# Kernel optimization log

Hardware: AMD Instinct MI355X
Metric: run time of the kernel (lower is better)

## Reference

```python
import jax, jax.numpy as jnp
import numpy as np

N_FFT = 1024
HOP = 256
B = 8
T = 2048  # n_frames
FREQ = N_FFT // 2 + 1


def setup_inputs() -> dict:
    key = jax.random.key(0)
    k1, k2 = jax.random.split(key)
    real_stft = jax.random.normal(k1, (B, 1, T, FREQ), dtype=jnp.float32)
    imag_stft = jax.random.normal(k2, (B, 1, T, FREQ), dtype=jnp.float32)
    # Build DFT synthesis matrices (same as torch module __init__, scaled=False)
    n = np.arange(N_FFT)
    hann = (0.5 - 0.5 * np.cos(2.0 * np.pi * n / N_FFT))  # fftbins=True hann
    ang = 2.0 * np.pi * np.outer(n, n) / N_FFT            # [k, n]
    W_real = (np.cos(ang) * hann[None, :] / N_FFT).astype(np.float32)
    W_imag = (np.sin(ang) * hann[None, :] / N_FFT).astype(np.float32)
    ola_window = (hann ** 2).astype(np.float32)
    return {
        "real_stft": real_stft,
        "imag_stft": imag_stft,
        "W_real": jnp.asarray(W_real),
        "W_imag": jnp.asarray(W_imag),
        "ola_window": jnp.asarray(ola_window),
    }


def reference(real_stft, imag_stft, W_real, W_imag, ola_window):
    n_fft = W_real.shape[0]
    b, _, n_frames, _ = real_stft.shape
    # (B, T, F) -> (B, F, T)
    fr = jnp.swapaxes(real_stft[:, 0], 1, 2)
    fi = jnp.swapaxes(imag_stft[:, 0], 1, 2)
    # Hermitian extension to full spectrum (B, n_fft, T)
    full_r = jnp.concatenate([fr, jnp.flip(fr[:, 1:-1, :], axis=1)], axis=1)
    full_i = jnp.concatenate([fi, -jnp.flip(fi[:, 1:-1, :], axis=1)], axis=1)
    # 1x1-conv DFT projection: out[b,t,n] = sum_k W[k,n] * x[b,k,t]
    frames = (jnp.einsum('kn,bkt->btn', W_real, full_r)
              - jnp.einsum('kn,bkt->btn', W_imag, full_i))  # (B, T, n_fft)
    out_len = (n_frames - 1) * HOP + n_fft
    # Overlap-add fold via scatter-add
    idx = (jnp.arange(n_frames)[:, None] * HOP + jnp.arange(n_fft)[None, :]).reshape(-1)
    y = jnp.zeros((b, out_len), frames.dtype).at[:, idx].add(frames.reshape(b, -1))
    # Window-sum fold + normalization
    wsum = jnp.zeros((out_len,), frames.dtype).at[idx].add(jnp.tile(ola_window, n_frames))
    wsum = jnp.clip(wsum, 1e-11, None)
    y = y / wsum[None, :]
    half = n_fft // 2
    return y[:, half:out_len - half]
```

## Files before the change

### kernel.cpp

```cpp
#include <hip/hip_runtime.h>


#define BATCH    8
#define NFRAMES  2048
#define FREQ     513
#define OUTCOLS  524032
#define FRAMES_B ((size_t)16384 * 1024 * 2)
#define TW_OFF   FRAMES_B
#define HANN_OFF (FRAMES_B + 16384)
#define WS_NEED  (FRAMES_B + 16384 + 4096)

typedef __attribute__((ext_vector_type(2))) float f32x2;
typedef __attribute__((ext_vector_type(4))) float f32x4;
typedef __attribute__((ext_vector_type(2))) unsigned uint2v;

__device__ __forceinline__ unsigned short f2bf(float x) {
    unsigned u = __float_as_uint(x);
    return (unsigned short)((u + 0x7fffu + ((u >> 16) & 1u)) >> 16);
}

__device__ __forceinline__ f32x2 cmul(f32x2 u, f32x4 w4) {
    return (f32x2){u[0], u[0]} * (f32x2){w4[0], w4[1]}
         + (f32x2){u[1], u[1]} * (f32x2){w4[2], w4[3]};
}

__global__ __launch_bounds__(256) void table_prep(const float* __restrict__ ola,
                                                  float* __restrict__ tw4,
                                                  float* __restrict__ hann) {
    int k = blockIdx.x * 256 + threadIdx.x;
    float s, c;
    sincosf(6.283185307179586f * (float)k * (1.0f / 1024.0f), &s, &c);
    ((f32x4*)tw4)[k] = (f32x4){c, s, -s, c};
    hann[k] = sqrtf(ola[k]) * (1.0f / 1024.0f);
}

__global__ __launch_bounds__(64, 4) void ifft_wave(
    const float* __restrict__ re, const float* __restrict__ im,
    const float* __restrict__ twg, const float* __restrict__ hann,
    unsigned short* __restrict__ frames) {
    __shared__ f32x2 L[1088];

    const int l  = threadIdx.x;
    const int r0 = blockIdx.x * 2;
    const f32x4* tw4 = (const f32x4*)twg;

    const float* fre0 = re + (size_t)r0 * FREQ;
    const float* fim0 = im + (size_t)r0 * FREQ;
    const float* fre1 = fre0 + FREQ;
    const float* fim1 = fim0 + FREQ;

#define BFLY(IA, IB, IC, ID, T1, O0, O1, O2, O3)                              \
    {                                                                         \
        f32x2 apc = (IA) + (IC), amc = (IA) - (IC);                           \
        f32x2 bpd = (IB) + (ID), bmd = (IB) - (ID);                           \
        f32x2 jb  = (f32x2){-bmd[1], bmd[0]};                    \
        O0 = apc + bpd;                                                       \
        O1 = cmul(amc + jb, w1##T1);                                          \
        O2 = cmul(apc - bpd, w2##T1);                                         \
        O3 = cmul(amc - jb, w3##T1);                                          \
    }

    f32x2 s1[4][4];
#pragma unroll
    for (int j = 0; j < 4; ++j) {
        f32x2 in[4];
#pragma unroll
        for (int k = 0; k < 4; ++k) {
            int n  = l + 64 * j + 256 * k;
            int mm = (n <= 512) ? n : (1024 - n);
            float A1 = fre0[mm], B1 = fim0[mm];
            float A2 = fre1[mm], B2 = fim1[mm];
            if (n == 0 || n == 512) { B1 = 0.0f; B2 = 0.0f; }
            in[k] = (n <= 512) ? (f32x2){A1 - B2, B1 + A2}
                               : (f32x2){A1 + B2, A2 - B1};
        }
        const int t1 = l + 64 * j;
        f32x4 w1A = tw4[t1], w2A = tw4[2 * t1], w3A = tw4[3 * t1];
        BFLY(in[0], in[1], in[2], in[3], A, s1[j][0], s1[j][1], s1[j][2], s1[j][3]);
    }

    {
        const int t1 = 4 * l;
        f32x4 w1B = tw4[t1], w2B = tw4[2 * t1], w3B = tw4[3 * t1];
#pragma unroll
        for (int r = 0; r < 4; ++r) {
            f32x2 o0, o1, o2, o3;
            BFLY(s1[0][r], s1[1][r], s1[2][r], s1[3][r], B, o0, o1, o2, o3);
            int n0 = 16 * l + r;
            L[n0      + (n0 >> 4)]        = o0;
            L[n0 + 4  + ((n0 + 4) >> 4)]  = o1;
            L[n0 + 8  + ((n0 + 8) >> 4)]  = o2;
            L[n0 + 12 + ((n0 + 12) >> 4)] = o3;
        }
    }
    __syncthreads();

    f32x2 s3[4][4];
#pragma unroll
    for (int j = 0; j < 4; ++j) {
        f32x2 in[4];
#pragma unroll
        for (int k = 0; k < 4; ++k) {
            int n = l + 64 * j + 256 * k;
            in[k] = L[n + (n >> 4)];
        }
        const int t1 = ((l + 64 * j) >> 4) << 4;
        f32x4 w1C = tw4[t1], w2C = tw4[2 * t1], w3C = tw4[3 * t1];
        BFLY(in[0], in[1], in[2], in[3], C, s3[j][0], s3[j][1], s3[j][2], s3[j][3]);
    }
    __syncthreads();

    {
        const int t1 = (l >> 4) << 6;
        f32x4 w1D = tw4[t1], w2D = tw4[2 * t1], w3D = tw4[3 * t1];
#pragma unroll
        for (int r = 0; r < 4; ++r) {
            f32x2 o0, o1, o2, o3;
            BFLY(s3[0][r], s3[1][r], s3[2][r], s3[3][r], D, o0, o1, o2, o3);
            int n0 = 256 * (l >> 4) + 16 * r + (l & 15);
            int n1 = n0 + 64, n2 = n0 + 128, n3 = n0 + 192;
            L[n0 + (n0 >> 4)] = o0;
            L[n1 + (n1 >> 4)] = o1;
            L[n2 + (n2 >> 4)] = o2;
            L[n3 + (n3 >> 4)] = o3;
        }
    }
    __syncthreads();

    unsigned short* fR = frames + (size_t)r0 * 1024;
    unsigned short* fI = fR + 1024;
#pragma unroll
    for (int h = 0; h < 4; ++h) {
        int n0 = l + 64 * h;
        int n1 = n0 + 256, n2 = n0 + 512, n3 = n0 + 768;
        f32x2 a = L[n0 + (n0 >> 4)];
        f32x2 b = L[n1 + (n1 >> 4)];
        f32x2 c = L[n2 + (n2 >> 4)];
        f32x2 d = L[n3 + (n3 >> 4)];
        f32x2 apc = a + c, amc = a - c, bpd = b + d, bmd = b - d;
        f32x2 jb  = (f32x2){-bmd[1], bmd[0]};
        f32x2 y0 = apc + bpd, y1 = amc + jb, y2 = apc - bpd, y3 = amc - jb;
        float h0 = hann[n0], h1 = hann[n1], h2 = hann[n2], h3 = hann[n3];
        fR[n0] = f2bf(y0[0] * h0);  fI[n0] = f2bf(y0[1] * h0);
        fR[n1] = f2bf(y1[0] * h1);  fI[n1] = f2bf(y1[1] * h1);
        fR[n2] = f2bf(y2[0] * h2);  fI[n2] = f2bf(y2[1] * h2);
        fR[n3] = f2bf(y3[0] * h3);  fI[n3] = f2bf(y3[1] * h3);
    }
#undef BFLY
}

__global__ __launch_bounds__(256) void ola_fold4(
    const unsigned short* __restrict__ frames, const float* __restrict__ ola,
    float* __restrict__ out) {
    const int col0 = (blockIdx.x * 256 + threadIdx.x) * 4;
    if (col0 >= OUTCOLS) return;
    const int b  = blockIdx.y;
    const int s  = col0 + 512;
    const int g  = s >> 8;
    const int ls = s & 255;

    float a0 = 0.f, a1 = 0.f, a2 = 0.f, a3 = 0.f;
    float w0 = 0.f, w1 = 0.f, w2 = 0.f, w3 = 0.f;
#pragma unroll
    for (int j = 0; j < 4; ++j) {
        const int t = g - j;
        if (t >= 0 && t < NFRAMES) {
            uint2v u = *(const uint2v*)(frames + (((size_t)(b * NFRAMES + t)) << 10) + ls + 256 * j);
            a0 += __uint_as_float(u[0] << 16);
            a1 += __uint_as_float(u[0] & 0xffff0000u);
            a2 += __uint_as_float(u[1] << 16);
            a3 += __uint_as_float(u[1] & 0xffff0000u);
            f32x4 o = *(const f32x4*)(ola + ls + 256 * j);
            w0 += o[0]; w1 += o[1]; w2 += o[2]; w3 += o[3];
        }
    }
    f32x4 r = (f32x4){a0 / fmaxf(w0, 1e-11f), a1 / fmaxf(w1, 1e-11f),
                      a2 / fmaxf(w2, 1e-11f), a3 / fmaxf(w3, 1e-11f)};
    *(f32x4*)(out + (size_t)b * OUTCOLS + col0) = r;
}

__global__ __launch_bounds__(256) void istft_naive(
    const float* __restrict__ re, const float* __restrict__ im,
    const float* __restrict__ Wr, const float* __restrict__ Wi,
    const float* __restrict__ ola, float* __restrict__ out) {
    const int g = blockIdx.x + 2, b = blockIdx.y, ls = threadIdx.x;
    __shared__ float s_fr[4][FREQ];
    __shared__ float s_fi[4][FREQ];
#pragma unroll
    for (int jj = 0; jj < 4; ++jj) {
        const int t = g - jj;
        const bool valid = (t >= 0 && t < NFRAMES);
        const size_t base = ((size_t)b * NFRAMES + (valid ? t : 0)) * FREQ;
        for (int k = ls; k < FREQ; k += 256) {
            const float f = (k == 0 || k == FREQ - 1) ? 1.0f : 2.0f;
            s_fr[jj][k] = valid ? re[base + k] * f : 0.0f;
            s_fi[jj][k] = valid ? im[base + k] * f : 0.0f;
        }
    }
    __syncthreads();
    const float* wr = Wr + ls;
    const float* wi = Wi + ls;
    float acc = 0.0f;
    for (int k = 0; k < FREQ; ++k) {
        const float* wrk = wr + (size_t)k * 1024;
        const float* wik = wi + (size_t)k * 1024;
#pragma unroll
        for (int jj = 0; jj < 4; ++jj) {
            acc = fmaf(wrk[jj * 256], s_fr[jj][k], acc);
            acc = fmaf(-wik[jj * 256], s_fi[jj][k], acc);
        }
    }
    float wsv = 0.0f;
#pragma unroll
    for (int jj = 0; jj < 4; ++jj) {
        const int t = g - jj;
        if (t >= 0 && t < NFRAMES) wsv += ola[ls + jj * 256];
    }
    wsv = fmaxf(wsv, 1e-11f);
    out[(size_t)b * OUTCOLS + (g * 256 + ls - 512)] = acc / wsv;
}

extern "C" void kernel_launch(void* const* d_in, const int* in_sizes, int n_in,
                              void* d_out, int out_size, void* d_ws, size_t ws_size,
                              hipStream_t stream) {
    const float* re  = (const float*)d_in[0];
    const float* im  = (const float*)d_in[1];
    const float* Wr  = (const float*)d_in[2];
    const float* Wi  = (const float*)d_in[3];
    const float* ola = (const float*)d_in[4];
    float* out = (float*)d_out;

    if (ws_size >= WS_NEED) {
        unsigned short* frames = (unsigned short*)d_ws;
        float* tw   = (float*)((char*)d_ws + TW_OFF);
        float* hann = (float*)((char*)d_ws + HANN_OFF);
        hipLaunchKernelGGL(table_prep, dim3(4), dim3(256), 0, stream, ola, tw, hann);
        hipLaunchKernelGGL(ifft_wave, dim3(8192), dim3(64), 0, stream,
                           re, im, tw, hann, frames);
        hipLaunchKernelGGL(ola_fold4, dim3(512, BATCH), dim3(256), 0, stream,
                           frames, ola, out);
    } else {
        dim3 grid(2047, BATCH);
        hipLaunchKernelGGL(istft_naive, grid, dim3(256), 0, stream,
                           re, im, Wr, Wi, ola, out);
    }
}
```

Measured before the change: 42.06 us.

## Fuse twiddle table into FFT kernel with 4 waves per block and wave-local LDS

Drops the table_prep launch and computes twiddles inline with fast sincos plus angle-doubling recurrences, and computes the hann scale from ola inside the FFT. Packs four independent wavefronts per 256-thread block, each with its own LDS slice, and replaces __syncthreads with a wave-local waitcnt plus sched barrier. The LDS exchange now moves real and imaginary planes separately using float4 stores and padded strides. This removes one kernel launch, global table loads and block barriers, at the cost of extra transcendental ALU work and slightly lower twiddle accuracy from __sincosf.

```diff
diff --git a/kernel.cpp b/kernel.cpp
--- a/kernel.cpp
+++ b/kernel.cpp
@@ -6,9 +6,7 @@
 #define FREQ     513
 #define OUTCOLS  524032
 #define FRAMES_B ((size_t)16384 * 1024 * 2)
-#define TW_OFF   FRAMES_B
-#define HANN_OFF (FRAMES_B + 16384)
-#define WS_NEED  (FRAMES_B + 16384 + 4096)
+#define WS_NEED  FRAMES_B
 
 typedef __attribute__((ext_vector_type(2))) float f32x2;
 typedef __attribute__((ext_vector_type(4))) float f32x4;
@@ -19,48 +17,42 @@
     return (unsigned short)((u + 0x7fffu + ((u >> 16) & 1u)) >> 16);
 }
 
-__device__ __forceinline__ f32x2 cmul(f32x2 u, f32x4 w4) {
-    return (f32x2){u[0], u[0]} * (f32x2){w4[0], w4[1]}
-         + (f32x2){u[1], u[1]} * (f32x2){w4[2], w4[3]};
-}
-
-__global__ __launch_bounds__(256) void table_prep(const float* __restrict__ ola,
-                                                  float* __restrict__ tw4,
-                                                  float* __restrict__ hann) {
-    int k = blockIdx.x * 256 + threadIdx.x;
-    float s, c;
-    sincosf(6.283185307179586f * (float)k * (1.0f / 1024.0f), &s, &c);
-    ((f32x4*)tw4)[k] = (f32x4){c, s, -s, c};
-    hann[k] = sqrtf(ola[k]) * (1.0f / 1024.0f);
-}
-
-__global__ __launch_bounds__(64, 4) void ifft_wave(
-    const float* __restrict__ re, const float* __restrict__ im,
-    const float* __restrict__ twg, const float* __restrict__ hann,
-    unsigned short* __restrict__ frames) {
-    __shared__ f32x2 L[1088];
-
-    const int l  = threadIdx.x;
-    const int r0 = blockIdx.x * 2;
-    const f32x4* tw4 = (const f32x4*)twg;
-
-    const float* fre0 = re + (size_t)r0 * FREQ;
-    const float* fim0 = im + (size_t)r0 * FREQ;
-    const float* fre1 = fre0 + FREQ;
-    const float* fim1 = fim0 + FREQ;
+#define DSYNC() do { asm volatile("s_waitcnt lgkmcnt(0)" ::: "memory"); \
+                     __builtin_amdgcn_sched_barrier(0); } while (0)
 
 #define BFLY(IA, IB, IC, ID, T1, O0, O1, O2, O3)                              \
     {                                                                         \
         f32x2 apc = (IA) + (IC), amc = (IA) - (IC);                           \
         f32x2 bpd = (IB) + (ID), bmd = (IB) - (ID);                           \
         f32x2 jb  = (f32x2){-bmd[1], bmd[0]};                    \
+        float s1_, c1_;                                                       \
+        __sincosf((float)(T1) * 6.135923151542565e-3f, &s1_, &c1_);           \
+        float c2_ = fmaf(-2.0f * s1_, s1_, 1.0f), s2_ = 2.0f * s1_ * c1_;     \
+        float c3_ = c2_ * c1_ - s2_ * s1_, s3_ = s2_ * c1_ + c2_ * s1_;       \
+        f32x2 u1 = amc + jb, u2 = apc - bpd, u3 = amc - jb;                   \
         O0 = apc + bpd;                                                       \
-        O1 = cmul(amc + jb, w1##T1);                                          \
-        O2 = cmul(apc - bpd, w2##T1);                                         \
-        O3 = cmul(amc - jb, w3##T1);                                          \
-    }
-
-    f32x2 s1[4][4];
+        O1 = (f32x2){u1[0] * c1_ - u1[1] * s1_, u1[0] * s1_ + u1[1] * c1_};   \
+        O2 = (f32x2){u2[0] * c2_ - u2[1] * s2_, u2[0] * s2_ + u2[1] * c2_};   \
+        O3 = (f32x2){u3[0] * c3_ - u3[1] * s3_, u3[0] * s3_ + u3[1] * c3_};   \
+    }
+
+__global__ __launch_bounds__(256, 5) void ifft_wave4(
+    const float* __restrict__ re, const float* __restrict__ im,
+    const float* __restrict__ ola, unsigned short* __restrict__ frames) {
+    __shared__ float L[4][1052];
+
+    const int tid = threadIdx.x;
+    const int l   = tid & 63;
+    const int w   = tid >> 6;
+    const int r0  = (blockIdx.x * 4 + w) * 2;
+    float* P = &L[w][0];
+
+    const float* fre0 = re + (size_t)r0 * FREQ;
+    const float* fim0 = im + (size_t)r0 * FREQ;
+    const float* fre1 = fre0 + FREQ;
+    const float* fim1 = fim0 + FREQ;
+
+    f32x2 s1v[4][4];
 #pragma unroll
     for (int j = 0; j < 4; ++j) {
         f32x2 in[4];
@@ -74,79 +66,117 @@
             in[k] = (n <= 512) ? (f32x2){A1 - B2, B1 + A2}
                                : (f32x2){A1 + B2, A2 - B1};
         }
-        const int t1 = l + 64 * j;
-        f32x4 w1A = tw4[t1], w2A = tw4[2 * t1], w3A = tw4[3 * t1];
-        BFLY(in[0], in[1], in[2], in[3], A, s1[j][0], s1[j][1], s1[j][2], s1[j][3]);
-    }
-
-    {
-        const int t1 = 4 * l;
-        f32x4 w1B = tw4[t1], w2B = tw4[2 * t1], w3B = tw4[3 * t1];
-#pragma unroll
-        for (int r = 0; r < 4; ++r) {
-            f32x2 o0, o1, o2, o3;
-            BFLY(s1[0][r], s1[1][r], s1[2][r], s1[3][r], B, o0, o1, o2, o3);
-            int n0 = 16 * l + r;
-            L[n0      + (n0 >> 4)]        = o0;
-            L[n0 + 4  + ((n0 + 4) >> 4)]  = o1;
-            L[n0 + 8  + ((n0 + 8) >> 4)]  = o2;
-            L[n0 + 12 + ((n0 + 12) >> 4)] = o3;
-        }
-    }
-    __syncthreads();
-
-    f32x2 s3[4][4];
+        BFLY(in[0], in[1], in[2], in[3], l + 64 * j,
+             s1v[j][0], s1v[j][1], s1v[j][2], s1v[j][3]);
+    }
+
+    f32x4 wRe[4], wIm[4];
+#pragma unroll
+    for (int r = 0; r < 4; ++r) {
+        f32x2 o0, o1, o2, o3;
+        BFLY(s1v[0][r], s1v[1][r], s1v[2][r], s1v[3][r], 4 * l, o0, o1, o2, o3);
+        wRe[0][r] = o0[0]; wIm[0][r] = o0[1];
+        wRe[1][r] = o1[0]; wIm[1][r] = o1[1];
+        wRe[2][r] = o2[0]; wIm[2][r] = o2[1];
+        wRe[3][r] = o3[0]; wIm[3][r] = o3[1];
+    }
+
+    {
+        const int wb = 16 * l + 8 * (l >> 4);
+#pragma unroll
+        for (int k = 0; k < 4; ++k) *(f32x4*)&P[wb + 4 * k] = wRe[k];
+    }
+    DSYNC();
+    float rr[4][4], ri[4][4];
+#pragma unroll
+    for (int j = 0; j < 4; ++j)
+#pragma unroll
+        for (int k = 0; k < 4; ++k) rr[j][k] = P[l + 64 * j + 264 * k];
+    DSYNC();
+    {
+        const int wb = 16 * l + 8 * (l >> 4);
+#pragma unroll
+        for (int k = 0; k < 4; ++k) *(f32x4*)&P[wb + 4 * k] = wIm[k];
+    }
+    DSYNC();
+#pragma unroll
+    for (int j = 0; j < 4; ++j)
+#pragma unroll
+        for (int k = 0; k < 4; ++k) ri[j][k] = P[l + 64 * j + 264 * k];
+    DSYNC();
+
+    f32x2 s3v[4][4];
 #pragma unroll
     for (int j = 0; j < 4; ++j) {
-        f32x2 in[4];
-#pragma unroll
-        for (int k = 0; k < 4; ++k) {
-            int n = l + 64 * j + 256 * k;
-            in[k] = L[n + (n >> 4)];
-        }
-        const int t1 = ((l + 64 * j) >> 4) << 4;
-        f32x4 w1C = tw4[t1], w2C = tw4[2 * t1], w3C = tw4[3 * t1];
-        BFLY(in[0], in[1], in[2], in[3], C, s3[j][0], s3[j][1], s3[j][2], s3[j][3]);
-    }
-    __syncthreads();
-
-    {
-        const int t1 = (l >> 4) << 6;
-        f32x4 w1D = tw4[t1], w2D = tw4[2 * t1], w3D = tw4[3 * t1];
-#pragma unroll
-        for (int r = 0; r < 4; ++r) {
-            f32x2 o0, o1, o2, o3;
-            BFLY(s3[0][r], s3[1][r], s3[2][r], s3[3][r], D, o0, o1, o2, o3);
-            int n0 = 256 * (l >> 4) + 16 * r + (l & 15);
-            int n1 = n0 + 64, n2 = n0 + 128, n3 = n0 + 192;
-            L[n0 + (n0 >> 4)] = o0;
-            L[n1 + (n1 >> 4)] = o1;
-            L[n2 + (n2 >> 4)] = o2;
-            L[n3 + (n3 >> 4)] = o3;
-        }
-    }
-    __syncthreads();
+        f32x2 a = (f32x2){rr[j][0], ri[j][0]};
+        f32x2 b = (f32x2){rr[j][1], ri[j][1]};
+        f32x2 c = (f32x2){rr[j][2], ri[j][2]};
+        f32x2 d = (f32x2){rr[j][3], ri[j][3]};
+        BFLY(a, b, c, d, (((l + 64 * j) >> 4) << 4),
+             s3v[j][0], s3v[j][1], s3v[j][2], s3v[j][3]);
+    }
+
+    float eRe[4][4], eIm[4][4];
+#pragma unroll
+    for (int r = 0; r < 4; ++r) {
+        f32x2 o0, o1, o2, o3;
+        BFLY(s3v[0][r], s3v[1][r], s3v[2][r], s3v[3][r], ((l >> 4) << 6),
+             o0, o1, o2, o3);
+        eRe[0][r] = o0[0]; eIm[0][r] = o0[1];
+        eRe[1][r] = o1[0]; eIm[1][r] = o1[1];
+        eRe[2][r] = o2[0]; eIm[2][r] = o2[1];
+        eRe[3][r] = o3[0]; eIm[3][r] = o3[1];
+    }
+
+    {
+        const int wb = 256 * (l >> 4) + (l & 15) + 8 * (l >> 4);
+#pragma unroll
+        for (int k = 0; k < 4; ++k)
+#pragma unroll
+            for (int r = 0; r < 4; ++r) P[wb + 16 * r + 64 * k] = eRe[k][r];
+    }
+    DSYNC();
+    float yR[4][4], yI[4][4];
+#pragma unroll
+    for (int h = 0; h < 4; ++h)
+#pragma unroll
+        for (int k = 0; k < 4; ++k) yR[h][k] = P[l + 64 * h + 264 * k];
+    DSYNC();
+    {
+        const int wb = 256 * (l >> 4) + (l & 15) + 8 * (l >> 4);
+#pragma unroll
+        for (int k = 0; k < 4; ++k)
+#pragma unroll
+            for (int r = 0; r < 4; ++r) P[wb + 16 * r + 64 * k] = eIm[k][r];
+    }
+    DSYNC();
+#pragma unroll
+    for (int h = 0; h < 4; ++h)
+#pragma unroll
+        for (int k = 0; k < 4; ++k) yI[h][k] = P[l + 64 * h + 264 * k];
+    DSYNC();
 
     unsigned short* fR = frames + (size_t)r0 * 1024;
     unsigned short* fI = fR + 1024;
 #pragma unroll
     for (int h = 0; h < 4; ++h) {
-        int n0 = l + 64 * h;
-        int n1 = n0 + 256, n2 = n0 + 512, n3 = n0 + 768;
-        f32x2 a = L[n0 + (n0 >> 4)];
-        f32x2 b = L[n1 + (n1 >> 4)];
-        f32x2 c = L[n2 + (n2 >> 4)];
-        f32x2 d = L[n3 + (n3 >> 4)];
+        f32x2 a = (f32x2){yR[h][0], yI[h][0]};
+        f32x2 b = (f32x2){yR[h][1], yI[h][1]};
+        f32x2 c = (f32x2){yR[h][2], yI[h][2]};
+        f32x2 d = (f32x2){yR[h][3], yI[h][3]};
         f32x2 apc = a + c, amc = a - c, bpd = b + d, bmd = b - d;
         f32x2 jb  = (f32x2){-bmd[1], bmd[0]};
         f32x2 y0 = apc + bpd, y1 = amc + jb, y2 = apc - bpd, y3 = amc - jb;
-        float h0 = hann[n0], h1 = hann[n1], h2 = hann[n2], h3 = hann[n3];
-        fR[n0] = f2bf(y0[0] * h0);  fI[n0] = f2bf(y0[1] * h0);
-        fR[n1] = f2bf(y1[0] * h1);  fI[n1] = f2bf(y1[1] * h1);
-        fR[n2] = f2bf(y2[0] * h2);  fI[n2] = f2bf(y2[1] * h2);
-        fR[n3] = f2bf(y3[0] * h3);  fI[n3] = f2bf(y3[1] * h3);
-    }
-#undef BFLY
+        int n0 = l + 64 * h;
+        float h0 = sqrtf(ola[n0])       * (1.0f / 1024.0f);
+        float h1 = sqrtf(ola[n0 + 256]) * (1.0f / 1024.0f);
+        float h2 = sqrtf(ola[n0 + 512]) * (1.0f / 1024.0f);
+        float h3 = sqrtf(ola[n0 + 768]) * (1.0f / 1024.0f);
+        fR[n0]       = f2bf(y0[0] * h0);  fI[n0]       = f2bf(y0[1] * h0);
+        fR[n0 + 256] = f2bf(y1[0] * h1);  fI[n0 + 256] = f2bf(y1[1] * h1);
+        fR[n0 + 512] = f2bf(y2[0] * h2);  fI[n0 + 512] = f2bf(y2[1] * h2);
+        fR[n0 + 768] = f2bf(y3[0] * h3);  fI[n0 + 768] = f2bf(y3[1] * h3);
+    }
 }
 
 __global__ __launch_bounds__(256) void ola_fold4(
@@ -232,11 +262,8 @@
 
     if (ws_size >= WS_NEED) {
         unsigned short* frames = (unsigned short*)d_ws;
-        float* tw   = (float*)((char*)d_ws + TW_OFF);
-        float* hann = (float*)((char*)d_ws + HANN_OFF);
-        hipLaunchKernelGGL(table_prep, dim3(4), dim3(256), 0, stream, ola, tw, hann);
-        hipLaunchKernelGGL(ifft_wave, dim3(8192), dim3(64), 0, stream,
-                           re, im, tw, hann, frames);
+        hipLaunchKernelGGL(ifft_wave4, dim3(2048), dim3(256), 0, stream,
+                           re, im, ola, frames);
         hipLaunchKernelGGL(ola_fold4, dim3(512, BATCH), dim3(256), 0, stream,
                            frames, ola, out);
     } else {
```

Measured after the change: 37.48 us. 1.12x faster.
